# Performance work log

Measured on AMD Instinct MI355X. Metric: run time of the kernel, lower is better.

The kernel has to match this reference:

```python
import jax, jax.numpy as jnp
import numpy as np
from jax import lax

B, H, W, C = 16, 56, 56, 256
NH = 8
KD = C // NH  # key/head dim = 32
FF = 1024
EPS = 1e-6
SCALE = KD ** -0.5


def _layernorm(x, g, b):
    m = jnp.mean(x, axis=-1, keepdims=True)
    v = jnp.mean(jnp.square(x - m), axis=-1, keepdims=True)
    return (x - m) * lax.rsqrt(v + EPS) * g + b


def _dwconv(x, w, b):
    # x: (B,H,W,Cd), w: (kh,kw,1,Cd) depthwise (groups = Cd), stride 1, SAME padding
    return lax.conv_general_dilated(
        x, w, window_strides=(1, 1), padding='SAME',
        dimension_numbers=('NHWC', 'HWIO', 'NHWC'),
        feature_group_count=x.shape[-1]) + b


def setup_inputs() -> dict:
    key = jax.random.key(0)
    ks = jax.random.split(key, 20)
    r = lambda i, shape, s=0.02: jax.random.normal(ks[i], shape, jnp.float32) * s
    return {
        'x': jax.random.normal(ks[0], (B, H, W, C), jnp.float32),
        'mask_h': jax.random.normal(ks[1], (NH, H, H), jnp.float32),
        'mask_w': jax.random.normal(ks[2], (NH, W, W), jnp.float32),
        # pos: DWConv2d(C, 3, 1, 1)
        'pos_w': r(3, (3, 3, 1, C)), 'pos_b': jnp.zeros((C,), jnp.float32),
        # retention layer norm
        'ln1_g': jnp.ones((C,), jnp.float32), 'ln1_b': jnp.zeros((C,), jnp.float32),
        # MaSA projections (stored as (in, out) so y = x @ W + b)
        'q_w': r(4, (C, C)), 'q_b': jnp.zeros((C,), jnp.float32),
        'k_w': r(5, (C, C)), 'k_b': jnp.zeros((C,), jnp.float32),
        'v_w': r(6, (C, C)), 'v_b': jnp.zeros((C,), jnp.float32),
        # lepe: DWConv2d(C, 5, 1, 2)
        'lepe_w': r(7, (5, 5, 1, C)), 'lepe_b': jnp.zeros((C,), jnp.float32),
        'out_w': r(8, (C, C)), 'out_b': jnp.zeros((C,), jnp.float32),
        # final layer norm
        'ln2_g': jnp.ones((C,), jnp.float32), 'ln2_b': jnp.zeros((C,), jnp.float32),
        # FFN
        'fc1_w': r(9, (C, FF)), 'fc1_b': jnp.zeros((FF,), jnp.float32),
        'fc2_w': r(10, (FF, C)), 'fc2_b': jnp.zeros((C,), jnp.float32),
    }


def _masa(x, mask_h, mask_w, q_w, q_b, k_w, k_b, v_w, v_b, lepe_w, lepe_b, out_w, out_b):
    b, h, w, _ = x.shape
    q = x @ q_w + q_b
    k = (x @ k_w + k_b) * SCALE
    v = x @ v_w + v_b
    lepe = _dwconv(v, lepe_w, lepe_b)
    qh = q.reshape(b, h, w, NH, KD)
    kh = k.reshape(b, h, w, NH, KD)
    vh = v.reshape(b, h, w, NH, KD)
    # width-axis retention: scores (b, h, NH, w, w), mask_w broadcasts as (NH, w, w)
    attn_w = jax.nn.softmax(jnp.einsum('bhqnd,bhknd->bhnqk', qh, kh) + mask_w, axis=-1)
    vw = jnp.einsum('bhnqk,bhknd->bhnqd', attn_w, vh)  # (b, h, NH, w, KD)
    # height-axis retention: scores (b, w, NH, h, h), mask_h broadcasts as (NH, h, h)
    attn_h = jax.nn.softmax(jnp.einsum('bqwnd,bkwnd->bwnqk', qh, kh) + mask_h, axis=-1)
    out = jnp.einsum('bwnqk,bknwd->bqwnd', attn_h, vw)  # (b, h, w, NH, KD)
    out = out.reshape(b, h, w, NH * KD) + lepe
    return out @ out_w + out_b


def reference(x, mask_h, mask_w, pos_w, pos_b, ln1_g, ln1_b,
              q_w, q_b, k_w, k_b, v_w, v_b, lepe_w, lepe_b, out_w, out_b,
              ln2_g, ln2_b, fc1_w, fc1_b, fc2_w, fc2_b):
    # RetBlock (retention='whole', no layerscale, no dropout / drop_path)
    x = x + _dwconv(x, pos_w, pos_b)
    x = x + _masa(_layernorm(x, ln1_g, ln1_b), mask_h, mask_w,
                  q_w, q_b, k_w, k_b, v_w, v_b, lepe_w, lepe_b, out_w, out_b)
    y = _layernorm(x, ln2_g, ln2_b)
    y = jax.nn.gelu(y @ fc1_w + fc1_b, approximate=False) @ fc2_w + fc2_b
    return x + y
```

## Files before the change

### kernel.cpp

```cpp
#include <hip/hip_runtime.h>
#include <hip/hip_bf16.h>
#include <math.h>
#include <stdint.h>

typedef __bf16 bf16;
typedef __bf16 bf16x8 __attribute__((ext_vector_type(8)));
typedef __bf16 bf16x4 __attribute__((ext_vector_type(4)));
typedef float f32x4 __attribute__((ext_vector_type(4)));

#define AS1 __attribute__((address_space(1)))
#define AS3 __attribute__((address_space(3)))

#define NPIX (16*56*56)
#define CH 256
#define SCALE_K 0.17677669529663687f

__device__ __forceinline__ float gelu_fast(float vv) {
    float t = vv * (-2.30220781f + -0.10294330f * vv * vv);
    float e = __builtin_amdgcn_exp2f(t);
    return vv * __builtin_amdgcn_rcpf(1.0f + e);
}

__global__ __launch_bounds__(256) void prep_kernel(
    const float* __restrict__ q_w, const float* __restrict__ k_w,
    const float* __restrict__ v_w, const float* __restrict__ out_w,
    const float* __restrict__ fc1_w, const float* __restrict__ fc2_w,
    const float* __restrict__ qb, const float* __restrict__ kb,
    const float* __restrict__ vb,
    bf16* __restrict__ wt_qkv, bf16* __restrict__ wt_out,
    bf16* __restrict__ wt_fc1, bf16* __restrict__ wt_fc2,
    float* __restrict__ qkvb)
{
    int idx = blockIdx.x * 256 + threadIdx.x;
    if (idx < 262144) {
        int w = idx >> 16;
        int j = idx & 65535;
        int n = j >> 8, k = j & 255;
        const float* src = (w == 0) ? q_w : (w == 1) ? k_w : (w == 2) ? v_w : out_w;
        float scale = (w == 1) ? SCALE_K : 1.0f;
        bf16* dst = (w < 3) ? (wt_qkv + w * 65536) : wt_out;
        dst[j] = (bf16)(src[k * 256 + n] * scale);
    } else if (idx < 524288) {
        int j = idx - 262144;
        int n = j >> 8, k = j & 255;
        wt_fc1[j] = (bf16)(fc1_w[k * 1024 + n]);
    } else if (idx < 786432) {
        int j = idx - 524288;
        int n = j >> 10, k = j & 1023;
        wt_fc2[j] = (bf16)(fc2_w[k * 256 + n]);
    } else if (idx < 787200) {
        int i = idx - 786432;
        qkvb[i] = (i < 256) ? qb[i] : (i < 512) ? kb[i - 256] * SCALE_K : vb[i - 512];
    }
}

__global__ __launch_bounds__(256) void posconv_ln_kernel(
    const float* __restrict__ x, const float* __restrict__ w,
    const float* __restrict__ bias, const float* __restrict__ g,
    const float* __restrict__ bta, float* __restrict__ x1,
    bf16* __restrict__ tln)
{
    const int wave = threadIdx.x >> 6, lane = threadIdx.x & 63;
    const long pix = (long)blockIdx.x * 4 + wave;
    const int ww = (int)(pix % 56);
    const int hh = (int)((pix / 56) % 56);
    const int b  = (int)(pix / 3136);
    const int c  = lane * 4;
    float4 acc = ((const float4*)(bias + c))[0];
    float4 xin = ((const float4*)(x + pix * 256 + c))[0];
    acc.x += xin.x; acc.y += xin.y; acc.z += xin.z; acc.w += xin.w;
    #pragma unroll
    for (int dh = 0; dh < 3; ++dh) {
        int h2 = hh + dh - 1;
        if (h2 < 0 || h2 >= 56) continue;
        #pragma unroll
        for (int dw = 0; dw < 3; ++dw) {
            int w2 = ww + dw - 1;
            if (w2 < 0 || w2 >= 56) continue;
            float4 xv = ((const float4*)(x + (((long)(b * 56 + h2)) * 56 + w2) * 256 + c))[0];
            float4 wv = ((const float4*)(w + (dh * 3 + dw) * 256 + c))[0];
            acc.x += xv.x * wv.x; acc.y += xv.y * wv.y;
            acc.z += xv.z * wv.z; acc.w += xv.w * wv.w;
        }
    }
    ((float4*)(x1 + pix * 256 + c))[0] = acc;
    float s  = acc.x + acc.y + acc.z + acc.w;
    float q2 = acc.x * acc.x + acc.y * acc.y + acc.z * acc.z + acc.w * acc.w;
    #pragma unroll
    for (int o = 32; o; o >>= 1) {
        s  += __shfl_xor(s,  o, 64);
        q2 += __shfl_xor(q2, o, 64);
    }
    float mean = s * (1.0f / 256.0f);
    float var  = q2 * (1.0f / 256.0f) - mean * mean;
    float rs   = rsqrtf(var + 1e-6f);
    float4 gv = ((const float4*)g)[lane];
    float4 bv = ((const float4*)bta)[lane];
    bf16* o4 = tln + pix * 256 + c;
    o4[0] = (bf16)((acc.x - mean) * rs * gv.x + bv.x);
    o4[1] = (bf16)((acc.y - mean) * rs * gv.y + bv.y);
    o4[2] = (bf16)((acc.z - mean) * rs * gv.z + bv.z);
    o4[3] = (bf16)((acc.w - mean) * rs * gv.w + bv.w);
}

__global__ __launch_bounds__(256) void lepe_kernel(
    const bf16* __restrict__ vpl, const float* __restrict__ w,
    const float* __restrict__ bias, bf16* __restrict__ out)
{
    long idx = (long)blockIdx.x * 256 + threadIdx.x;
    int c8 = (int)(idx & 31);
    long pix = idx >> 5;
    int ww = (int)(pix % 56);
    int hh = (int)((pix / 56) % 56);
    int b  = (int)(pix / 3136);
    int c  = c8 * 8;
    float acc[8];
    #pragma unroll
    for (int j = 0; j < 8; ++j) acc[j] = bias[c + j];
    #pragma unroll
    for (int dh = 0; dh < 5; ++dh) {
        int h2 = hh + dh - 2;
        if (h2 < 0 || h2 >= 56) continue;
        #pragma unroll
        for (int dw = 0; dw < 5; ++dw) {
            int w2 = ww + dw - 2;
            if (w2 < 0 || w2 >= 56) continue;
            bf16x8 vv = *(const bf16x8*)(vpl + (((long)(b * 56 + h2)) * 56 + w2) * 256 + c);
            const float4* wp = (const float4*)(w + (dh * 5 + dw) * 256 + c);
            float4 w0 = wp[0], w1 = wp[1];
            acc[0] += (float)vv[0] * w0.x; acc[1] += (float)vv[1] * w0.y;
            acc[2] += (float)vv[2] * w0.z; acc[3] += (float)vv[3] * w0.w;
            acc[4] += (float)vv[4] * w1.x; acc[5] += (float)vv[5] * w1.y;
            acc[6] += (float)vv[6] * w1.z; acc[7] += (float)vv[7] * w1.w;
        }
    }
    bf16* o = out + pix * 256 + c;
    #pragma unroll
    for (int j = 0; j < 8; ++j) o[j] = (bf16)acc[j];
}

template<bool WIDTH>
__global__ __launch_bounds__(256) void attn_mfma_kernel(
    const bf16* __restrict__ qp, const bf16* __restrict__ kp,
    const bf16* __restrict__ vsrc, const float* __restrict__ mask,
    const bf16* __restrict__ lepe, bf16* __restrict__ outp)
{
    __shared__ bf16 VtAll[4][32][72];
    __shared__ bf16 PlAll[4][16][72];
    const int tid = threadIdx.x;
    const int wave = tid >> 6, lane = tid & 63;
    const int g = lane >> 4, ql = lane & 15;
    const int n  = blockIdx.x / 224;
    const int s  = (blockIdx.x % 224) * 4 + wave;
    const int b  = s / 56, rc = s % 56;
    bf16 (*Vt)[72] = VtAll[wave];
    bf16 (*Pl)[72] = PlAll[wave];
    const long basePix = WIDTH ? ((long)(b * 56 + rc)) * 56 : (long)b * 3136 + rc;
    const long pixStride = WIDTH ? 1 : 56;
    const long stride = pixStride * 256;
    const bf16* qb = qp + basePix * 256 + n * 32;
    const bf16* kb = kp + basePix * 256 + n * 32;
    const bf16* vbp = vsrc + basePix * 256 + n * 32;

    #pragma unroll
    for (int it = 0; it < 2; ++it) {
        int idx = it * 64 + lane;
        if (idx < 112) {
            int pp = idx >> 2, chunk = idx & 3;
            int pos0 = pp * 2;
            bf16x8 v0 = *(const bf16x8*)(vbp + (long)pos0 * stride + chunk * 8);
            bf16x8 v1 = *(const bf16x8*)(vbp + (long)(pos0 + 1) * stride + chunk * 8);
            int colb = pos0 ^ (chunk << 3);
            #pragma unroll
            for (int j = 0; j < 8; ++j) {
                union { bf16 h[2]; unsigned int u; } pk;
                pk.h[0] = v0[j]; pk.h[1] = v1[j];
                *(unsigned int*)&Vt[chunk * 8 + j][colb] = pk.u;
            }
        }
    }
    if (lane < 32) {
        int d = lane;
        int colb = 56 ^ ((d >> 3) << 3);
        *(float4*)&Vt[d][colb] = (float4){0.f, 0.f, 0.f, 0.f};
    }

    bf16x8 qf[4], kf[4];
    #pragma unroll
    for (int t4 = 0; t4 < 4; ++t4) {
        int row = ql + 16 * t4; if (row > 55) row = 55;
        qf[t4] = *(const bf16x8*)(qb + (long)row * stride + 8 * g);
        kf[t4] = *(const bf16x8*)(kb + (long)row * stride + 8 * g);
    }

    f32x4 sA[4][4];
    #pragma unroll
    for (int qt = 0; qt < 4; ++qt)
        #pragma unroll
        for (int kt = 0; kt < 4; ++kt)
            sA[qt][kt] = __builtin_amdgcn_mfma_f32_16x16x32_bf16(
                kf[kt], qf[qt], (f32x4){0.f, 0.f, 0.f, 0.f}, 0, 0, 0);

    const float* mrow = mask + n * 3136;
    #pragma unroll
    for (int qt = 0; qt < 4; ++qt) {
        int qm = ql + 16 * qt; if (qm > 55) qm = 55;
        #pragma unroll
        for (int kt = 0; kt < 4; ++kt) {
            if (kt == 3 && g >= 2) {
                sA[qt][3][0] = -3.0e38f; sA[qt][3][1] = -3.0e38f;
                sA[qt][3][2] = -3.0e38f; sA[qt][3][3] = -3.0e38f;
            } else {
                float4 mv = *(const float4*)(mrow + qm * 56 + kt * 16 + 4 * g);
                sA[qt][kt][0] += mv.x; sA[qt][kt][1] += mv.y;
                sA[qt][kt][2] += mv.z; sA[qt][kt][3] += mv.w;
            }
        }
    }

    #pragma unroll
    for (int qt = 0; qt < 4; ++qt) {
        float m = -3.0e38f;
        #pragma unroll
        for (int kt = 0; kt < 4; ++kt)
            #pragma unroll
            for (int r = 0; r < 4; ++r) m = fmaxf(m, sA[qt][kt][r]);
        m = fmaxf(m, __shfl_xor(m, 16, 64));
        m = fmaxf(m, __shfl_xor(m, 32, 64));
        float p[4][4];
        float sum = 0.f;
        #pragma unroll
        for (int kt = 0; kt < 4; ++kt)
            #pragma unroll
            for (int r = 0; r < 4; ++r) {
                float e = exp2f((sA[qt][kt][r] - m) * 1.4426950408889634f);
                p[kt][r] = e; sum += e;
            }
        sum += __shfl_xor(sum, 16, 64);
        sum += __shfl_xor(sum, 32, 64);
        float rinv = 1.0f / sum;
        #pragma unroll
        for (int kt = 0; kt < 4; ++kt) {
            bf16x4 w;
            #pragma unroll
            for (int r = 0; r < 4; ++r) w[r] = (bf16)(p[kt][r] * rinv);
            *(bf16x4*)&Pl[ql][kt * 16 + 4 * g] = w;
        }
        #pragma unroll
        for (int nt = 0; nt < 2; ++nt) {
            f32x4 o = {0.f, 0.f, 0.f, 0.f};
            #pragma unroll
            for (int ks = 0; ks < 2; ++ks) {
                bf16x8 af = *(const bf16x8*)&Pl[ql][ks * 32 + 8 * g];
                int vrow = ql + 16 * nt;
                int vcol = (ks * 32 + 8 * g) ^ ((vrow >> 3) << 3);
                bf16x8 bv = *(const bf16x8*)&Vt[vrow][vcol];
                o = __builtin_amdgcn_mfma_f32_16x16x32_bf16(af, bv, o, 0, 0, 0);
            }
            if (!(qt == 3 && g >= 2)) {
                #pragma unroll
                for (int r = 0; r < 4; ++r) {
                    int q = 16 * qt + 4 * g + r;
                    long addr = (basePix + (long)q * pixStride) * 256 + n * 32 + nt * 16 + ql;
                    float vv = o[r];
                    if (!WIDTH) vv += (float)lepe[addr];
                    outp[addr] = (bf16)vv;
                }
            }
        }
    }
}

template<bool GELU, bool RESID, bool OUT_BF16, bool QKV3>
__global__ __launch_bounds__(256) void gemm_kernel(
    const bf16* __restrict__ A, const bf16* __restrict__ Wt,
    const float* __restrict__ bias, const float* __restrict__ resid,
    void* __restrict__ Cout, int M, int N, int K)
{
    __shared__ bf16 As[128 * 64];
    __shared__ bf16 Bs[128 * 64];
    const int t = threadIdx.x;
    const int wave = t >> 6, lane = t & 63;
    const int nTilesN = N >> 7;
    const int q8 = gridDim.x >> 3;
    const int o = ((int)blockIdx.x & 7) * q8 + ((int)blockIdx.x >> 3);
    const int tm = o / nTilesN, tn = o % nTilesN;
    const long m0 = (long)tm * 128, n0 = (long)tn * 128;
    const int waveM = (wave >> 1) * 64, waveN = (wave & 1) * 64;
    f32x4 acc[4][4] = {};

    for (int k0 = 0; k0 < K; k0 += 64) {
        #pragma unroll
        for (int i = 0; i < 4; ++i) {
            int c = i * 256 + wave * 64 + lane;
            int r = c >> 3, cc = (c & 7) * 8;
            const bf16* ga = A  + (m0 + r) * (long)K + k0 + cc;
            const bf16* gb = Wt + (n0 + r) * (long)K + k0 + cc;
            __builtin_amdgcn_global_load_lds(
                (const AS1 void*)ga,
                (AS3 void*)(As + (i * 256 + wave * 64) * 8), 16, 0, 0);
            __builtin_amdgcn_global_load_lds(
                (const AS1 void*)gb,
                (AS3 void*)(Bs + (i * 256 + wave * 64) * 8), 16, 0, 0);
        }
        __syncthreads();
        #pragma unroll
        for (int kk = 0; kk < 2; ++kk) {
            bf16x8 af[4], bfr[4];
            const int krow = kk * 32 + (lane >> 4) * 8;
            #pragma unroll
            for (int fm = 0; fm < 4; ++fm)
                af[fm] = *(const bf16x8*)&As[(waveM + fm * 16 + (lane & 15)) * 64 + krow];
            #pragma unroll
            for (int fn = 0; fn < 4; ++fn)
                bfr[fn] = *(const bf16x8*)&Bs[(waveN + fn * 16 + (lane & 15)) * 64 + krow];
            #pragma unroll
            for (int fm = 0; fm < 4; ++fm)
                #pragma unroll
                for (int fn = 0; fn < 4; ++fn)
                    acc[fm][fn] = __builtin_amdgcn_mfma_f32_16x16x32_bf16(
                        af[fm], bfr[fn], acc[fm][fn], 0, 0, 0);
        }
        __syncthreads();
    }

    #pragma unroll
    for (int fm = 0; fm < 4; ++fm) {
        #pragma unroll
        for (int r = 0; r < 4; ++r) {
            const long m = m0 + waveM + fm * 16 + (lane >> 4) * 4 + r;
            #pragma unroll
            for (int fn = 0; fn < 4; ++fn) {
                const long n = n0 + waveN + fn * 16 + (lane & 15);
                float vv = acc[fm][fn][r] + bias[n];
                if (GELU)  vv = gelu_fast(vv);
                if (RESID) vv += resid[m * N + n];
                if (QKV3) {
                    long pl = n >> 8;
                    ((bf16*)Cout)[pl * (long)NPIX * 256 + m * 256 + (n & 255)] = (bf16)vv;
                } else if (OUT_BF16) {
                    ((bf16*)Cout)[m * N + n] = (bf16)vv;
                } else {
                    ((float*)Cout)[m * N + n] = vv;
                }
            }
        }
    }
}

__global__ __launch_bounds__(256) void outln_kernel(
    const bf16* __restrict__ A, const bf16* __restrict__ Wt,
    const float* __restrict__ bias, const float* __restrict__ resid,
    const float* __restrict__ g2, const float* __restrict__ b2,
    float* __restrict__ x2out, bf16* __restrict__ uout)
{
    __shared__ bf16 As[64 * 64];
    __shared__ bf16 Bs[256 * 64];
    const int t = threadIdx.x;
    const int wave = t >> 6, lane = t & 63;
    const int g = lane >> 4, ql = lane & 15;
    const int q8 = gridDim.x >> 3;
    const int o = ((int)blockIdx.x & 7) * q8 + ((int)blockIdx.x >> 3);
    const long m0 = (long)o * 64;
    const int waveM = wave * 16;
    f32x4 acc[16] = {};

    for (int k0 = 0; k0 < 256; k0 += 64) {
        #pragma unroll
        for (int i = 0; i < 2; ++i) {
            int c = i * 256 + wave * 64 + lane;
            int r = c >> 3, cc = (c & 7) * 8;
            const bf16* ga = A + (m0 + r) * 256 + k0 + cc;
            __builtin_amdgcn_global_load_lds(
                (const AS1 void*)ga,
                (AS3 void*)(As + (i * 256 + wave * 64) * 8), 16, 0, 0);
        }
        #pragma unroll
        for (int i = 0; i < 8; ++i) {
            int c = i * 256 + wave * 64 + lane;
            int r = c >> 3, cc = (c & 7) * 8;
            const bf16* gb = Wt + r * 256 + k0 + cc;
            __builtin_amdgcn_global_load_lds(
                (const AS1 void*)gb,
                (AS3 void*)(Bs + (i * 256 + wave * 64) * 8), 16, 0, 0);
        }
        __syncthreads();
        #pragma unroll
        for (int kk = 0; kk < 2; ++kk) {
            const int krow = kk * 32 + g * 8;
            bf16x8 af = *(const bf16x8*)&As[(waveM + ql) * 64 + krow];
            #pragma unroll
            for (int fn = 0; fn < 16; ++fn) {
                bf16x8 bv = *(const bf16x8*)&Bs[(fn * 16 + ql) * 64 + krow];
                acc[fn] = __builtin_amdgcn_mfma_f32_16x16x32_bf16(af, bv, acc[fn], 0, 0, 0);
            }
        }
        __syncthreads();
    }

    float rsum[4] = {}, rsq[4] = {};
    #pragma unroll
    for (int fn = 0; fn < 16; ++fn) {
        const int n = fn * 16 + ql;
        const float bn = bias[n];
        #pragma unroll
        for (int r = 0; r < 4; ++r) {
            const long m = m0 + waveM + g * 4 + r;
            float v = acc[fn][r] + bn + resid[m * 256 + n];
            acc[fn][r] = v;
            rsum[r] += v; rsq[r] += v * v;
        }
    }
    #pragma unroll
    for (int r = 0; r < 4; ++r) {
        float s = rsum[r], q = rsq[r];
        #pragma unroll
        for (int off = 8; off; off >>= 1) {
            s += __shfl_xor(s, off, 64);
            q += __shfl_xor(q, off, 64);
        }
        float mean = s * (1.0f / 256.0f);
        float var  = q * (1.0f / 256.0f) - mean * mean;
        rsum[r] = mean;
        rsq[r]  = rsqrtf(var + 1e-6f);
    }
    #pragma unroll
    for (int fn = 0; fn < 16; ++fn) {
        const int n = fn * 16 + ql;
        const float gn = g2[n], bn2 = b2[n];
        #pragma unroll
        for (int r = 0; r < 4; ++r) {
            const long m = m0 + waveM + g * 4 + r;
            float v = acc[fn][r];
            x2out[m * 256 + n] = v;
            uout[m * 256 + n] = (bf16)((v - rsum[r]) * rsq[r] * gn + bn2);
        }
    }
}

extern "C" void kernel_launch(void* const* d_in, const int* in_sizes, int n_in,
                              void* d_out, int out_size, void* d_ws, size_t ws_size,
                              hipStream_t stream)
{
    (void)in_sizes; (void)n_in; (void)out_size; (void)ws_size;
    const float* x      = (const float*)d_in[0];
    const float* mask_h = (const float*)d_in[1];
    const float* mask_w = (const float*)d_in[2];
    const float* pos_w  = (const float*)d_in[3];
    const float* pos_b  = (const float*)d_in[4];
    const float* ln1_g  = (const float*)d_in[5];
    const float* ln1_b  = (const float*)d_in[6];
    const float* q_w    = (const float*)d_in[7];
    const float* q_b    = (const float*)d_in[8];
    const float* k_w    = (const float*)d_in[9];
    const float* k_b    = (const float*)d_in[10];
    const float* v_w    = (const float*)d_in[11];
    const float* v_b    = (const float*)d_in[12];
    const float* lepe_w = (const float*)d_in[13];
    const float* lepe_b = (const float*)d_in[14];
    const float* out_w  = (const float*)d_in[15];
    const float* out_b  = (const float*)d_in[16];
    const float* ln2_g  = (const float*)d_in[17];
    const float* ln2_b  = (const float*)d_in[18];
    const float* fc1_w  = (const float*)d_in[19];
    const float* fc1_b  = (const float*)d_in[20];
    const float* fc2_w  = (const float*)d_in[21];
    const float* fc2_b  = (const float*)d_in[22];

    char* ws = (char*)d_ws;
    size_t off = 0;
    auto alloc = [&](size_t bytes) -> void* {
        void* p = ws + off;
        off += (bytes + 255) & ~(size_t)255;
        return p;
    };
    const int M = NPIX;
    float* x1     = (float*)alloc((size_t)M * 256 * 4);
    bf16*  tln    = (bf16*) alloc((size_t)M * 256 * 2);
    bf16*  qkv3   = (bf16*) alloc((size_t)M * 768 * 2);
    bf16*  lepeb  = (bf16*) alloc((size_t)M * 256 * 2);
    bf16*  vwb    = (bf16*) alloc((size_t)M * 256 * 2);
    bf16*  obuf   = (bf16*) alloc((size_t)M * 256 * 2);
    bf16*  wt_qkv = (bf16*) alloc((size_t)768 * 256 * 2);
    bf16*  wt_out = (bf16*) alloc((size_t)256 * 256 * 2);
    bf16*  wt_fc1 = (bf16*) alloc((size_t)1024 * 256 * 2);
    bf16*  wt_fc2 = (bf16*) alloc((size_t)256 * 1024 * 2);
    float* qkvb   = (float*)alloc(768 * 4);
    bf16*  qpl    = qkv3;
    bf16*  kpl    = qkv3 + (size_t)M * 256;
    bf16*  vpl    = qkv3 + (size_t)M * 512;
    bf16*  h1     = tln;
    float* outf   = (float*)d_out;

    prep_kernel<<<3075, 256, 0, stream>>>(
        q_w, k_w, v_w, out_w, fc1_w, fc2_w, q_b, k_b, v_b,
        wt_qkv, wt_out, wt_fc1, wt_fc2, qkvb);

    posconv_ln_kernel<<<12544, 256, 0, stream>>>(x, pos_w, pos_b, ln1_g, ln1_b, x1, tln);
    gemm_kernel<false, false, true, true><<<392 * 6, 256, 0, stream>>>(
        tln, wt_qkv, qkvb, nullptr, qkv3, M, 768, 256);
    lepe_kernel<<<6272, 256, 0, stream>>>(vpl, lepe_w, lepe_b, lepeb);
    attn_mfma_kernel<true><<<1792, 256, 0, stream>>>(qpl, kpl, vpl, mask_w, nullptr, vwb);
    attn_mfma_kernel<false><<<1792, 256, 0, stream>>>(qpl, kpl, vwb, mask_h, lepeb, obuf);
    outln_kernel<<<784, 256, 0, stream>>>(
        obuf, wt_out, out_b, x1, ln2_g, ln2_b, outf, lepeb);
    gemm_kernel<true, false, true, false><<<392 * 8, 256, 0, stream>>>(
        lepeb, wt_fc1, fc1_b, nullptr, h1, M, 1024, 256);
    gemm_kernel<false, true, false, false><<<392 * 2, 256, 0, stream>>>(
        h1, wt_fc2, fc2_b, outf, outf, M, 256, 1024);
}
```

Baseline: 416.5 us.

## Load GEMM operands directly from global into registers, dropping LDS staging

The tiled GEMM and the out-projection+LayerNorm kernel no longer stage A and B tiles through shared memory with global_load_lds and barriers. Each wave now loads its MFMA fragments straight from global memory, and K becomes a compile-time template parameter. This removes the LDS traffic and the __syncthreads calls. In exchange, operand reuse across waves now depends on L1/L2 caching, the fragment loads are strided and not coalesced, and memory latency is no longer hidden by a shared staging step.

```diff
diff --git a/kernel.cpp b/kernel.cpp
--- a/kernel.cpp
+++ b/kernel.cpp
@@ -271,16 +271,15 @@
     }
 }
 
-template<bool GELU, bool RESID, bool OUT_BF16, bool QKV3>
+template<bool GELU, bool RESID, bool OUT_BF16, bool QKV3, int KK>
 __global__ __launch_bounds__(256) void gemm_kernel(
     const bf16* __restrict__ A, const bf16* __restrict__ Wt,
     const float* __restrict__ bias, const float* __restrict__ resid,
-    void* __restrict__ Cout, int M, int N, int K)
-{
-    __shared__ bf16 As[128 * 64];
-    __shared__ bf16 Bs[128 * 64];
+    void* __restrict__ Cout, int M, int N)
+{
     const int t = threadIdx.x;
     const int wave = t >> 6, lane = t & 63;
+    const int g = lane >> 4, ql = lane & 15;
     const int nTilesN = N >> 7;
     const int q8 = gridDim.x >> 3;
     const int o = ((int)blockIdx.x & 7) * q8 + ((int)blockIdx.x >> 3);
@@ -289,39 +288,24 @@
     const int waveM = (wave >> 1) * 64, waveN = (wave & 1) * 64;
     f32x4 acc[4][4] = {};
 
-    for (int k0 = 0; k0 < K; k0 += 64) {
-        #pragma unroll
-        for (int i = 0; i < 4; ++i) {
-            int c = i * 256 + wave * 64 + lane;
-            int r = c >> 3, cc = (c & 7) * 8;
-            const bf16* ga = A  + (m0 + r) * (long)K + k0 + cc;
-            const bf16* gb = Wt + (n0 + r) * (long)K + k0 + cc;
-            __builtin_amdgcn_global_load_lds(
-                (const AS1 void*)ga,
-                (AS3 void*)(As + (i * 256 + wave * 64) * 8), 16, 0, 0);
-            __builtin_amdgcn_global_load_lds(
-                (const AS1 void*)gb,
-                (AS3 void*)(Bs + (i * 256 + wave * 64) * 8), 16, 0, 0);
-        }
-        __syncthreads();
-        #pragma unroll
-        for (int kk = 0; kk < 2; ++kk) {
-            bf16x8 af[4], bfr[4];
-            const int krow = kk * 32 + (lane >> 4) * 8;
-            #pragma unroll
-            for (int fm = 0; fm < 4; ++fm)
-                af[fm] = *(const bf16x8*)&As[(waveM + fm * 16 + (lane & 15)) * 64 + krow];
+    const bf16* Ab = A  + (m0 + waveM + ql) * (long)KK + g * 8;
+    const bf16* Bb = Wt + (n0 + waveN + ql) * (long)KK + g * 8;
+
+    #pragma unroll 2
+    for (int k0 = 0; k0 < KK; k0 += 32) {
+        bf16x8 af[4], bfr[4];
+        #pragma unroll
+        for (int fm = 0; fm < 4; ++fm)
+            af[fm] = *(const bf16x8*)(Ab + (long)(fm * 16) * KK + k0);
+        #pragma unroll
+        for (int fn = 0; fn < 4; ++fn)
+            bfr[fn] = *(const bf16x8*)(Bb + (long)(fn * 16) * KK + k0);
+        #pragma unroll
+        for (int fm = 0; fm < 4; ++fm)
             #pragma unroll
             for (int fn = 0; fn < 4; ++fn)
-                bfr[fn] = *(const bf16x8*)&Bs[(waveN + fn * 16 + (lane & 15)) * 64 + krow];
-            #pragma unroll
-            for (int fm = 0; fm < 4; ++fm)
-                #pragma unroll
-                for (int fn = 0; fn < 4; ++fn)
-                    acc[fm][fn] = __builtin_amdgcn_mfma_f32_16x16x32_bf16(
-                        af[fm], bfr[fn], acc[fm][fn], 0, 0, 0);
-        }
-        __syncthreads();
+                acc[fm][fn] = __builtin_amdgcn_mfma_f32_16x16x32_bf16(
+                    af[fm], bfr[fn], acc[fm][fn], 0, 0, 0);
     }
 
     #pragma unroll
@@ -354,8 +338,6 @@
     const float* __restrict__ g2, const float* __restrict__ b2,
     float* __restrict__ x2out, bf16* __restrict__ uout)
 {
-    __shared__ bf16 As[64 * 64];
-    __shared__ bf16 Bs[256 * 64];
     const int t = threadIdx.x;
     const int wave = t >> 6, lane = t & 63;
     const int g = lane >> 4, ql = lane & 15;
@@ -365,37 +347,16 @@
     const int waveM = wave * 16;
     f32x4 acc[16] = {};
 
-    for (int k0 = 0; k0 < 256; k0 += 64) {
-        #pragma unroll
-        for (int i = 0; i < 2; ++i) {
-            int c = i * 256 + wave * 64 + lane;
-            int r = c >> 3, cc = (c & 7) * 8;
-            const bf16* ga = A + (m0 + r) * 256 + k0 + cc;
-            __builtin_amdgcn_global_load_lds(
-                (const AS1 void*)ga,
-                (AS3 void*)(As + (i * 256 + wave * 64) * 8), 16, 0, 0);
-        }
-        #pragma unroll
-        for (int i = 0; i < 8; ++i) {
-            int c = i * 256 + wave * 64 + lane;
-            int r = c >> 3, cc = (c & 7) * 8;
-            const bf16* gb = Wt + r * 256 + k0 + cc;
-            __builtin_amdgcn_global_load_lds(
-                (const AS1 void*)gb,
-                (AS3 void*)(Bs + (i * 256 + wave * 64) * 8), 16, 0, 0);
-        }
-        __syncthreads();
-        #pragma unroll
-        for (int kk = 0; kk < 2; ++kk) {
-            const int krow = kk * 32 + g * 8;
-            bf16x8 af = *(const bf16x8*)&As[(waveM + ql) * 64 + krow];
-            #pragma unroll
-            for (int fn = 0; fn < 16; ++fn) {
-                bf16x8 bv = *(const bf16x8*)&Bs[(fn * 16 + ql) * 64 + krow];
-                acc[fn] = __builtin_amdgcn_mfma_f32_16x16x32_bf16(af, bv, acc[fn], 0, 0, 0);
-            }
-        }
-        __syncthreads();
+    const bf16* Ab = A  + (m0 + waveM + ql) * 256 + g * 8;
+    const bf16* Bb = Wt + ql * 256 + g * 8;
+
+    for (int k0 = 0; k0 < 256; k0 += 32) {
+        bf16x8 af = *(const bf16x8*)(Ab + k0);
+        #pragma unroll
+        for (int fn = 0; fn < 16; ++fn) {
+            bf16x8 bv = *(const bf16x8*)(Bb + (long)(fn * 16) * 256 + k0);
+            acc[fn] = __builtin_amdgcn_mfma_f32_16x16x32_bf16(af, bv, acc[fn], 0, 0, 0);
+        }
     }
 
     float rsum[4] = {}, rsq[4] = {};
@@ -497,15 +458,15 @@
         wt_qkv, wt_out, wt_fc1, wt_fc2, qkvb);
 
     posconv_ln_kernel<<<12544, 256, 0, stream>>>(x, pos_w, pos_b, ln1_g, ln1_b, x1, tln);
-    gemm_kernel<false, false, true, true><<<392 * 6, 256, 0, stream>>>(
-        tln, wt_qkv, qkvb, nullptr, qkv3, M, 768, 256);
+    gemm_kernel<false, false, true, true, 256><<<392 * 6, 256, 0, stream>>>(
+        tln, wt_qkv, qkvb, nullptr, qkv3, M, 768);
     lepe_kernel<<<6272, 256, 0, stream>>>(vpl, lepe_w, lepe_b, lepeb);
     attn_mfma_kernel<true><<<1792, 256, 0, stream>>>(qpl, kpl, vpl, mask_w, nullptr, vwb);
     attn_mfma_kernel<false><<<1792, 256, 0, stream>>>(qpl, kpl, vwb, mask_h, lepeb, obuf);
     outln_kernel<<<784, 256, 0, stream>>>(
         obuf, wt_out, out_b, x1, ln2_g, ln2_b, outf, lepeb);
-    gemm_kernel<true, false, true, false><<<392 * 8, 256, 0, stream>>>(
-        lepeb, wt_fc1, fc1_b, nullptr, h1, M, 1024, 256);
-    gemm_kernel<false, true, false, false><<<392 * 2, 256, 0, stream>>>(
-        h1, wt_fc2, fc2_b, outf, outf, M, 256, 1024);
-}
+    gemm_kernel<true, false, true, false, 256><<<392 * 8, 256, 0, stream>>>(
+        lepeb, wt_fc1, fc1_b, nullptr, h1, M, 1024);
+    gemm_kernel<false, true, false, false, 1024><<<392 * 2, 256, 0, stream>>>(
+        h1, wt_fc2, fc2_b, outf, outf, M, 256);
+}
```

New measurement: 602.7 us. 44.7% more time.
